# Performance work log

Hardware: AMD Instinct MI355X
Metric: run time of the kernel (lower is better)

Reference implementation:

```python
import jax, jax.numpy as jnp
from jax import lax
import numpy as np

# dims: T turns per dialogue, B dialogues, H = inpt_size (utter hidden), UE user embed,
# PE position embed, S = conv feature size, DEG avg in-degree
T, B, H, UE, PE, DEG = 30, 512, 256, 10, 16, 8
S = H + UE + PE          # 282, GRUCell(size, size)
OUT = 256                # context_hidden_size (output_size of linear2)
N = B * T                # merged graph nodes
E = N * DEG              # merged graph edges
LN_EPS = 1e-5


def _gru_cell(x, h, wih, whh, bih, bhh):
    # torch nn.GRUCell gate order: r, z, n
    gx = x @ wih.T + bih
    gh = h @ whh.T + bhh
    xr, xz, xn = jnp.split(gx, 3, axis=-1)
    hr, hz, hn = jnp.split(gh, 3, axis=-1)
    r = jax.nn.sigmoid(xr + hr)
    z = jax.nn.sigmoid(xz + hz)
    n = jnp.tanh(xn + r * hn)
    return (1.0 - z) * n + z * h


def _run_gru(xs, wih, whh, bih, bhh, reverse):
    # xs: [T, B, Din]; torch nn.GRU with zero initial hidden
    h0 = jnp.zeros((xs.shape[1], whh.shape[1]), xs.dtype)
    def step(h, x):
        hn = _gru_cell(x, h, wih, whh, bih, bhh)
        return hn, hn
    hT, ys = lax.scan(step, h0, xs, reverse=reverse)
    return ys, hT


def _forward(utter_hidden, ub, edge_weight,
             wih_f, whh_f, bih_f, bhh_f, wih_b, whh_b, bih_b, bhh_b,
             lin1_w, lin1_b, posemb,
             c1_wih, c1_whh, c1_bih, c1_bhh,
             c2_wih, c2_whh, c2_bih, c2_bhh,
             g1_w, g1_b, g2_w, g2_b, g3_w, g3_b,
             ln_g, ln_b, lin2_w, lin2_b, edge_index):
    # --- bidirectional GRU over turns + linear1 (GatedGCNContext.rnn) ---
    inp = jnp.concatenate([utter_hidden, ub], axis=-1)        # [T, B, H+UE]
    ys_f, h_f = _run_gru(inp, wih_f, whh_f, bih_f, bhh_f, False)
    ys_b, h_b = _run_gru(inp, wih_b, whh_b, bih_b, bhh_b, True)
    rnn_x = jnp.tanh(jnp.concatenate([ys_f, ys_b], -1) @ lin1_w.T + lin1_b)  # [T,B,H]
    # --- merged graph node features (PyG batching is batch-major) ---
    x0 = rnn_x.transpose(1, 0, 2).reshape(N, H)               # node b*T+t
    pos = posemb[jnp.tile(jnp.arange(T), B)]                  # [N, PE]
    ub_flat = ub.reshape(-1, UE)                              # faithful to original (turn-major)
    cell1 = (c1_wih, c1_whh, c1_bih, c1_bhh)
    cell2 = (c2_wih, c2_whh, c2_bih, c2_bhh)
    src, dst = edge_index[0], edge_index[1]

    def conv(xin, gw, gb):
        # message: edge_weight * GRUCell1(x_j, x_i); aggregate: scatter-add; update: Linear(GRUCell2(aggr, x))
        m = edge_weight[:, None] * _gru_cell(xin[src], xin[dst], *cell1)   # [E, S]
        aggr = jax.ops.segment_sum(m, dst, num_segments=N)                 # [N, S]
        return _gru_cell(aggr, xin, *cell2) @ gw.T + gb                    # [N, H]

    x1 = jnp.tanh(conv(jnp.concatenate([x0, pos, ub_flat], 1), g1_w, g1_b))
    x2 = jnp.tanh(conv(jnp.concatenate([x1, pos, ub_flat], 1), g2_w, g2_b))
    x3 = jnp.tanh(conv(jnp.concatenate([x2, pos, ub_flat], 1), g3_w, g3_b))
    xs = jnp.tanh(x1 + x2 + x3)
    mu = xs.mean(-1, keepdims=True)
    var = ((xs - mu) ** 2).mean(-1, keepdims=True)
    xs = ln_g * (xs - mu) / jnp.sqrt(var + LN_EPS) + ln_b     # LayerNorm (dropout = eval identity)
    gx = xs.reshape(B, T, H).transpose(1, 0, 2)               # chunk+stack+permute -> [T, B, H]
    out = jnp.tanh(jnp.concatenate([rnn_x, gx], -1) @ lin2_w.T + lin2_b)   # [T, B, OUT]
    return out


def setup_inputs() -> dict:
    key = jax.random.key(0)
    ks = iter(jax.random.split(key, 40))
    def p(shape):
        return jax.random.normal(next(ks), shape, dtype=jnp.float32) * 0.05
    # block-diagonal batched graph: per dialogue b, each node t receives DEG random in-edges
    rng = np.random.default_rng(0)
    off = (np.arange(B) * T)[:, None, None]
    src = rng.integers(0, T, size=(B, T, DEG)) + off
    dst = np.broadcast_to(np.arange(T)[None, :, None], (B, T, DEG)) + off
    edge_index = jnp.asarray(np.stack([src.ravel(), dst.ravel()]), dtype=jnp.int32)
    return {
        "utter_hidden": jax.random.normal(next(ks), (T, B, H), jnp.float32),
        "ub": jax.random.normal(next(ks), (T, B, UE), jnp.float32),
        "edge_weight": jax.random.uniform(next(ks), (E,), jnp.float32),
        "wih_f": p((3 * H, H + UE)), "whh_f": p((3 * H, H)), "bih_f": jnp.zeros((3 * H,)), "bhh_f": jnp.zeros((3 * H,)),
        "wih_b": p((3 * H, H + UE)), "whh_b": p((3 * H, H)), "bih_b": jnp.zeros((3 * H,)), "bhh_b": jnp.zeros((3 * H,)),
        "lin1_w": p((H, 2 * H)), "lin1_b": jnp.zeros((H,)),
        "posemb": p((100, PE)),
        "c1_wih": p((3 * S, S)), "c1_whh": p((3 * S, S)), "c1_bih": jnp.zeros((3 * S,)), "c1_bhh": jnp.zeros((3 * S,)),
        "c2_wih": p((3 * S, S)), "c2_whh": p((3 * S, S)), "c2_bih": jnp.zeros((3 * S,)), "c2_bhh": jnp.zeros((3 * S,)),
        "g1_w": p((H, S)), "g1_b": jnp.zeros((H,)),
        "g2_w": p((H, S)), "g2_b": jnp.zeros((H,)),
        "g3_w": p((H, S)), "g3_b": jnp.zeros((H,)),
        "ln_g": jnp.ones((H,)), "ln_b": jnp.zeros((H,)),
        "lin2_w": p((OUT, 2 * H)), "lin2_b": jnp.zeros((OUT,)),
        "edge_index": edge_index,
    }


def reference(utter_hidden, ub, edge_weight,
              wih_f, whh_f, bih_f, bhh_f, wih_b, whh_b, bih_b, bhh_b,
              lin1_w, lin1_b, posemb,
              c1_wih, c1_whh, c1_bih, c1_bhh,
              c2_wih, c2_whh, c2_bih, c2_bhh,
              g1_w, g1_b, g2_w, g2_b, g3_w, g3_b,
              ln_g, ln_b, lin2_w, lin2_b, edge_index):
    return _forward(utter_hidden, ub, edge_weight,
                    wih_f, whh_f, bih_f, bhh_f, wih_b, whh_b, bih_b, bhh_b,
                    lin1_w, lin1_b, posemb,
                    c1_wih, c1_whh, c1_bih, c1_bhh,
                    c2_wih, c2_whh, c2_bih, c2_bhh,
                    g1_w, g1_b, g2_w, g2_b, g3_w, g3_b,
                    ln_g, ln_b, lin2_w, lin2_b, edge_index)
```

## Files before the change

kernel.cpp:

```cpp
#include <hip/hip_runtime.h>
#include <math.h>

#define T_DIM 30
#define B_DIM 512
#define S_DIM 282
#define NB (T_DIM*B_DIM)
#define E_DIM (NB*8)
#define G3 846
#define GST 2538
#define KXP 288

typedef __attribute__((ext_vector_type(8))) short bf16x8;
typedef __attribute__((ext_vector_type(4))) float f32x4;

__device__ __forceinline__ float sigm(float x){ return 1.f/(1.f+expf(-x)); }

__device__ __forceinline__ ushort f2b(float f){
  union { float f; unsigned u; } v; v.f = f;
  unsigned r = v.u + 0x7fffu + ((v.u >> 16) & 1u);
  return (ushort)(r >> 16);
}
__device__ __forceinline__ float b2f(ushort b){
  union { unsigned u; float f; } v; v.u = ((unsigned)b) << 16; return v.f;
}
__device__ __forceinline__ void f2b2(float v, ushort& hi, ushort& lo){
  hi = f2b(v);
  lo = f2b(v - b2f(hi));
}

#define GLDS16(g, l) __builtin_amdgcn_global_load_lds( \
    (const __attribute__((address_space(1))) void*)(g), \
    (__attribute__((address_space(3))) void*)(l), 16, 0, 0)

__global__ __launch_bounds__(256, 2) void mfma_gemm3(
    const ushort* __restrict__ A, const ushort* __restrict__ W,
    const float* __restrict__ bias, float* __restrict__ C,
    int Nreal, int Kp, int ldc, int act, ushort* __restrict__ xout)
{
  __shared__ char smem[65536];

  int gx = gridDim.x;
  int h = blockIdx.y*gx + blockIdx.x;
  int nwg = gx*gridDim.y;
  int bx, by;
  if ((nwg & 7) == 0) {
    int q = nwg >> 3;
    int lwg = (h & 7)*q + (h >> 3);
    by = lwg / gx; bx = lwg - by*gx;
  } else { by = blockIdx.y; bx = blockIdx.x; }

  int tid  = threadIdx.x;
  int w    = tid >> 6;
  int lane = tid & 63;
  int lr = lane & 15;
  int lk = lane >> 4;
  int row0 = by*128;
  int col0 = bx*128;
  size_t astr = 2*(size_t)Kp;
  int NK = Kp >> 5;

  auto stage = [&](int buf, int kt){
    int kk = kt*32;
    char* Ab = smem + buf*32768;
    char* Wb = Ab + 16384;
    #pragma unroll
    for (int i = 0; i < 4; ++i) {
      int sb = w*256 + i*64;
      int s  = sb + lane;
      int r  = s >> 3;
      int rl = (s & 7) ^ (r & 7);
      int p  = rl >> 2, ks = rl & 3;
      const ushort* ga = A + (size_t)(row0 + r)*astr + (size_t)p*Kp + kk + ks*8;
      GLDS16(ga, Ab + sb*16);
      const ushort* gw = W + (size_t)(col0 + r)*astr + (size_t)p*Kp + kk + ks*8;
      GLDS16(gw, Wb + sb*16);
    }
  };
  auto rdfrag = [&](char* base, int r, int p)->bf16x8{
    int byte = r*128 + (((p*64) + lk*16) ^ ((r & 7) << 4));
    return *reinterpret_cast<const bf16x8*>(base + byte);
  };

  f32x4 acc[2][8] = {};
  stage(0, 0);
  __syncthreads();

  for (int kt = 0; kt < NK; ++kt) {
    int cur = kt & 1;
    if (kt + 1 < NK) stage(cur ^ 1, kt + 1);
    char* Ab = smem + cur*32768;
    char* Wb = Ab + 16384;

    bf16x8 a[2][2], b[8][2];
    #pragma unroll
    for (int i = 0; i < 2; ++i)
      #pragma unroll
      for (int p = 0; p < 2; ++p)
        a[i][p] = rdfrag(Ab, w*32 + i*16 + lr, p);
    #pragma unroll
    for (int j = 0; j < 8; ++j)
      #pragma unroll
      for (int p = 0; p < 2; ++p)
        b[j][p] = rdfrag(Wb, j*16 + lr, p);

    #pragma unroll
    for (int j = 0; j < 8; ++j) {
      acc[0][j] = __builtin_amdgcn_mfma_f32_16x16x32_bf16(a[0][0], b[j][0], acc[0][j], 0,0,0);
      acc[0][j] = __builtin_amdgcn_mfma_f32_16x16x32_bf16(a[0][1], b[j][0], acc[0][j], 0,0,0);
      acc[0][j] = __builtin_amdgcn_mfma_f32_16x16x32_bf16(a[0][0], b[j][1], acc[0][j], 0,0,0);
      acc[1][j] = __builtin_amdgcn_mfma_f32_16x16x32_bf16(a[1][0], b[j][0], acc[1][j], 0,0,0);
      acc[1][j] = __builtin_amdgcn_mfma_f32_16x16x32_bf16(a[1][1], b[j][0], acc[1][j], 0,0,0);
      acc[1][j] = __builtin_amdgcn_mfma_f32_16x16x32_bf16(a[1][0], b[j][1], acc[1][j], 0,0,0);
    }
    __syncthreads();
  }

  #pragma unroll
  for (int i = 0; i < 2; ++i) {
    #pragma unroll
    for (int j = 0; j < 8; ++j) {
      int cc = col0 + j*16 + lr;
      if (cc >= Nreal) continue;
      float bv = bias[cc];
      #pragma unroll
      for (int r = 0; r < 4; ++r) {
        int rr = row0 + w*32 + i*16 + lk*4 + r;
        float v = acc[i][j][r] + bv;
        if (act) v = tanhf(v);
        C[(size_t)rr*ldc + cc] = v;
        if (xout && cc < 256) {
          ushort hi, lo; f2b2(v, hi, lo);
          xout[(size_t)rr*2*KXP + cc]       = hi;
          xout[(size_t)rr*2*KXP + KXP + cc] = lo;
        }
      }
    }
  }
}

static inline void mgemm3(const ushort* A, const ushort* W, const float* bias,
                          float* C, int Nreal, int Npad, int Kp, int ldc,
                          int act, ushort* xout, hipStream_t s)
{
  dim3 grid((Npad + 127)/128, NB/128);
  mfma_gemm3<<<grid, 256, 0, s>>>(A, W, bias, C, Nreal, Kp, ldc, act, xout);
}

__global__ void cast_w(const float* __restrict__ w, ushort* __restrict__ wb,
                       int Nreal, int K, int Kp, int Npad)
{
  int idx = blockIdx.x*256 + threadIdx.x;
  if (idx >= Npad*Kp) return;
  int n = idx / Kp, k = idx - n*Kp;
  float v = (n < Nreal && k < K) ? w[(size_t)n*K + k] : 0.f;
  ushort hi, lo; f2b2(v, hi, lo);
  wb[(size_t)n*2*Kp + k]      = hi;
  wb[(size_t)n*2*Kp + Kp + k] = lo;
}
static inline void castw(const float* w, ushort* wb, int Nreal, int K, int Kp,
                         int Npad, hipStream_t s)
{
  int tot = Npad*Kp;
  cast_w<<<(tot+255)/256, 256, 0, s>>>(w, wb, Nreal, K, Kp, Npad);
}

__global__ void copy_f(const float* __restrict__ s, float* __restrict__ d, int n)
{
  int i = blockIdx.x*256 + threadIdx.x;
  if (i < n) d[i] = s[i];
}

__global__ void transpose_whh(const float* __restrict__ w, float* __restrict__ wt)
{
  int idx = blockIdx.x*256 + threadIdx.x;
  if (idx < 768*256) { int r = idx >> 8, c = idx & 255; wt[c*768 + r] = w[idx]; }
}

__global__ void build_inp(const float* __restrict__ utter, const float* __restrict__ ub,
                          ushort* __restrict__ inp)
{
  int r = blockIdx.x;
  for (int c = threadIdx.x; c < KXP; c += 128){
    float v = 0.f;
    if (c < 256)      v = utter[(size_t)r*256 + c];
    else if (c < 266) v = ub[(size_t)r*10 + (c-256)];
    ushort hi, lo; f2b2(v, hi, lo);
    inp[(size_t)r*2*KXP + c]       = hi;
    inp[(size_t)r*2*KXP + KXP + c] = lo;
  }
}

__global__ __launch_bounds__(256) void gru_step(
    const float* __restrict__ gx,
    const float* __restrict__ wtf, const float* __restrict__ bhh_f,
    const float* __restrict__ wtb, const float* __restrict__ bhh_b,
    float* __restrict__ ys_f, float* __restrict__ ys_b, int t)
{
  int dir = blockIdx.z;
  const float* wt  = dir ? wtb  : wtf;
  const float* bhh = dir ? bhh_b : bhh_f;
  float* ys = dir ? ys_b : ys_f;
  int tt = dir ? (T_DIM-1 - t) : t;
  const float* hprev = nullptr;
  if (t > 0) hprev = ys + (size_t)(dir ? tt+1 : tt-1) * B_DIM * 256;

  int tx = threadIdx.x & 63;
  int ty = threadIdx.x >> 6;
  int j = blockIdx.x * 64 + tx;
  int b = blockIdx.y * 4 + ty;

  __shared__ float sh[4][256];
  for (int i = threadIdx.x; i < 4*256; i += 256) {
    int bb = i >> 8, kk = i & 255;
    int gb = blockIdx.y*4 + bb;
    sh[bb][kk] = hprev ? hprev[(size_t)gb*256 + kk] : 0.f;
  }
  __syncthreads();

  float ar = bhh[j], az = bhh[256+j], an = bhh[512+j];
  for (int k = 0; k < 256; ++k) {
    float h = sh[ty][k];
    const float* wk = wt + (size_t)k*768;
    ar += h * wk[j];
    az += h * wk[256+j];
    an += h * wk[512+j];
  }
  size_t base = ((size_t)tt*B_DIM + b)*1536 + (size_t)dir*768;
  float r = sigm(gx[base + j]       + ar);
  float z = sigm(gx[base + 256 + j] + az);
  float n = tanhf(gx[base + 512 + j] + r*an);
  float h = sh[ty][j];
  ys[((size_t)tt*B_DIM + b)*256 + j] = (1.f - z)*n + z*h;
}

__global__ void build_cat(const float* __restrict__ a, const float* __restrict__ b2,
                          ushort* __restrict__ c, int mapmode)
{
  int r = blockIdx.x;
  int r2 = r;
  if (mapmode){ int t = r >> 9, bb = r & 511; r2 = bb*T_DIM + t; }
  for (int cix = threadIdx.x; cix < 512; cix += 128){
    float v = (cix < 256) ? a[(size_t)r*256 + cix] : b2[(size_t)r2*256 + (cix-256)];
    ushort hi, lo; f2b2(v, hi, lo);
    c[(size_t)r*1024 + cix]       = hi;
    c[(size_t)r*1024 + 512 + cix] = lo;
  }
}

__global__ void build_xin(const float* __restrict__ xsrc, int reorder,
                          const float* __restrict__ posemb, const float* __restrict__ ub,
                          ushort* __restrict__ xin)
{
  int n = blockIdx.x;
  int b = n / T_DIM, t = n % T_DIM;
  int srow = reorder ? (t*B_DIM + b) : n;
  for (int s = threadIdx.x; s < KXP; s += 128){
    float v = 0.f;
    if (s < 256)      v = xsrc[(size_t)srow*256 + s];
    else if (s < 272) v = posemb[t*16 + (s-256)];
    else if (s < 282) v = ub[(size_t)n*10 + (s-272)];
    ushort hi, lo; f2b2(v, hi, lo);
    xin[(size_t)n*2*KXP + s]       = hi;
    xin[(size_t)n*2*KXP + KXP + s] = lo;
  }
}

__global__ __launch_bounds__(128) void edge_aggr(
    const float* __restrict__ gate, const ushort* __restrict__ xin,
    const int* __restrict__ esrc, const int* __restrict__ edst,
    const float* __restrict__ ew, ushort* __restrict__ aggr)
{
  int e0 = blockIdx.x * 8;
  __shared__ int ssrc[8]; __shared__ float sw[8]; __shared__ int sdst;
  if (threadIdx.x < 8) { ssrc[threadIdx.x] = esrc[e0+threadIdx.x]; sw[threadIdx.x] = ew[e0+threadIdx.x]; }
  if (threadIdx.x == 0) sdst = edst[e0];
  __syncthreads();
  int i = sdst;
  for (int s = threadIdx.x; s < KXP; s += 128) {
    if (s >= S_DIM) {
      aggr[(size_t)i*2*KXP + s] = 0; aggr[(size_t)i*2*KXP + KXP + s] = 0; continue;
    }
    size_t gi = (size_t)i*GST;
    float hr = gate[gi + 846 + s];
    float hz = gate[gi + 1128 + s];
    float hn = gate[gi + 1410 + s];
    float hv = b2f(xin[(size_t)i*2*KXP + s]) + b2f(xin[(size_t)i*2*KXP + KXP + s]);
    float acc = 0.f;
    #pragma unroll
    for (int d = 0; d < 8; ++d) {
      size_t gj = (size_t)ssrc[d]*GST; float w = sw[d];
      float xr = gate[gj + s];
      float xz = gate[gj + 282 + s];
      float xn = gate[gj + 564 + s];
      float r = sigm(xr + hr);
      float z = sigm(xz + hz);
      float n = tanhf(xn + r*hn);
      acc += w * ((1.f - z)*n + z*hv);
    }
    ushort hi, lo; f2b2(acc, hi, lo);
    aggr[(size_t)i*2*KXP + s]       = hi;
    aggr[(size_t)i*2*KXP + KXP + s] = lo;
  }
}

__global__ __launch_bounds__(128) void gru2_combine(
    const float* __restrict__ gate, const ushort* __restrict__ xin,
    ushort* __restrict__ upd)
{
  int n = blockIdx.x;
  for (int s = threadIdx.x; s < KXP; s += 128) {
    if (s >= S_DIM) {
      upd[(size_t)n*2*KXP + s] = 0; upd[(size_t)n*2*KXP + KXP + s] = 0; continue;
    }
    size_t g = (size_t)n*GST;
    float xr = gate[g + 846 + s];
    float xz = gate[g + 1128 + s];
    float xn = gate[g + 1410 + s];
    float hr = gate[g + 1692 + s];
    float hz = gate[g + 1974 + s];
    float hn = gate[g + 2256 + s];
    float h  = b2f(xin[(size_t)n*2*KXP + s]) + b2f(xin[(size_t)n*2*KXP + KXP + s]);
    float r = sigm(xr + hr);
    float z = sigm(xz + hz);
    float nn = tanhf(xn + r*hn);
    ushort hi, lo; f2b2((1.f - z)*nn + z*h, hi, lo);
    upd[(size_t)n*2*KXP + s]       = hi;
    upd[(size_t)n*2*KXP + KXP + s] = lo;
  }
}

__global__ __launch_bounds__(256) void sum_ln(
    const float* __restrict__ x1, const float* __restrict__ x2, const float* __restrict__ x3,
    const float* __restrict__ g, const float* __restrict__ bta, float* __restrict__ out)
{
  int n = blockIdx.x; int j = threadIdx.x;
  size_t idx = (size_t)n*256 + j;
  float v = tanhf(x1[idx] + x2[idx] + x3[idx]);
  float s = v, sq = v*v;
  #pragma unroll
  for (int o = 32; o; o >>= 1) { s += __shfl_down(s, o, 64); sq += __shfl_down(sq, o, 64); }
  __shared__ float wsm[4], ws2[4];
  int lane = j & 63, w = j >> 6;
  if (lane == 0){ wsm[w] = s; ws2[w] = sq; }
  __syncthreads();
  float mean = (wsm[0]+wsm[1]+wsm[2]+wsm[3]) * (1.f/256.f);
  float m2   = (ws2[0]+ws2[1]+ws2[2]+ws2[3]) * (1.f/256.f);
  float var = m2 - mean*mean;
  float inv = rsqrtf(var + 1e-5f);
  out[idx] = g[j]*(v-mean)*inv + bta[j];
}

extern "C" void kernel_launch(void* const* d_in, const int* in_sizes, int n_in,
                              void* d_out, int out_size, void* d_ws, size_t ws_size,
                              hipStream_t stream)
{
  const float* utter = (const float*)d_in[0];
  const float* ub    = (const float*)d_in[1];
  const float* ew    = (const float*)d_in[2];
  const float* wih_f = (const float*)d_in[3];
  const float* whh_f = (const float*)d_in[4];
  const float* bih_f = (const float*)d_in[5];
  const float* bhh_f = (const float*)d_in[6];
  const float* wih_b = (const float*)d_in[7];
  const float* whh_b = (const float*)d_in[8];
  const float* bih_b = (const float*)d_in[9];
  const float* bhh_b = (const float*)d_in[10];
  const float* lin1_w= (const float*)d_in[11];
  const float* lin1_b= (const float*)d_in[12];
  const float* posemb= (const float*)d_in[13];
  const float* c1_wih= (const float*)d_in[14];
  const float* c1_whh= (const float*)d_in[15];
  const float* c1_bih= (const float*)d_in[16];
  const float* c1_bhh= (const float*)d_in[17];
  const float* c2_wih= (const float*)d_in[18];
  const float* c2_whh= (const float*)d_in[19];
  const float* c2_bih= (const float*)d_in[20];
  const float* c2_bhh= (const float*)d_in[21];
  const float* gw[3] = {(const float*)d_in[22], (const float*)d_in[24], (const float*)d_in[26]};
  const float* gb[3] = {(const float*)d_in[23], (const float*)d_in[25], (const float*)d_in[27]};
  const float* ln_g  = (const float*)d_in[28];
  const float* ln_b  = (const float*)d_in[29];
  const float* lin2_w= (const float*)d_in[30];
  const float* lin2_b= (const float*)d_in[31];
  const int*   eidx  = (const int*)d_in[32];
  const int* esrc = eidx;
  const int* edst = eidx + E_DIM;
  (void)ws_size; (void)n_in; (void)in_sizes; (void)out_size;

  float* ws = (float*)d_ws;
  size_t o = 0;
  auto A  = [&](size_t n){ size_t r = o; o += (n+3)&~(size_t)3; return r; };
  auto AU = [&](size_t n){ return A((n+1)/2); };

  size_t bGATE = A((size_t)NB*GST);
  size_t bYF   = A((size_t)NB*256);
  size_t bYB   = A((size_t)NB*256);
  size_t bRNN  = A((size_t)NB*256);
  size_t bBT   = A(2560);
  size_t bBX   = A(1536);
  size_t bB2   = A(896);
  size_t uXIN = AU((size_t)NB*2*KXP);
  size_t uAGG = AU((size_t)NB*2*KXP);
  size_t uWC1 = AU((size_t)2560*2*KXP);
  size_t uWXP = AU((size_t)1536*2*KXP);
  size_t uW2X = AU((size_t)896*2*KXP);
  size_t uG0  = AU((size_t)256*2*KXP);
  size_t uG1  = AU((size_t)256*2*KXP);
  size_t uG2  = AU((size_t)256*2*KXP);
  size_t uL1  = AU((size_t)256*2*512);
  size_t uL2  = AU((size_t)256*2*512);

  ushort* us = (ushort*)d_ws;
  auto U = [&](size_t fo){ return us + fo*2; };
  float* gate = ws + bGATE;
  float* wtf = gate + 23592960;
  float* wtb = wtf + 196608;
  ushort* uINP  = (ushort*)(ws + bYF);
  ushort* uCAT  = (ushort*)gate;
  float*  x3    = gate;

  castw(wih_f,  U(uWXP),                       768, 266,  KXP, 768, stream);
  castw(wih_b,  U(uWXP) + (size_t)768*2*KXP,   768, 266,  KXP, 768, stream);
  castw(c1_wih, U(uWC1),                       846, S_DIM, KXP, 846, stream);
  castw(c1_whh, U(uWC1) + (size_t)846*2*KXP,   846, S_DIM, KXP, 846, stream);
  castw(c2_whh, U(uWC1) + (size_t)1692*2*KXP,  846, S_DIM, KXP, 868, stream);
  castw(c2_wih, U(uW2X),                       846, S_DIM, KXP, 896, stream);
  castw(gw[0],  U(uG0), 256, S_DIM, KXP, 256, stream);
  castw(gw[1],  U(uG1), 256, S_DIM, KXP, 256, stream);
  castw(gw[2],  U(uG2), 256, S_DIM, KXP, 256, stream);
  castw(lin1_w, U(uL1), 256, 512, 512, 256, stream);
  castw(lin2_w, U(uL2), 256, 512, 512, 256, stream);
  const ushort* uGW[3] = {U(uG0), U(uG1), U(uG2)};
  copy_f<<<(846+255)/256,256,0,stream>>>(c1_bih, ws+bBT,        846);
  copy_f<<<(846+255)/256,256,0,stream>>>(c1_bhh, ws+bBT+846,    846);
  copy_f<<<(846+255)/256,256,0,stream>>>(c2_bhh, ws+bBT+1692,   846);
  copy_f<<<(768+255)/256,256,0,stream>>>(bih_f,  ws+bBX,        768);
  copy_f<<<(768+255)/256,256,0,stream>>>(bih_b,  ws+bBX+768,    768);
  copy_f<<<(846+255)/256,256,0,stream>>>(c2_bih, ws+bB2,        846);

  transpose_whh<<<(768*256+255)/256, 256, 0, stream>>>(whh_f, wtf);
  transpose_whh<<<(768*256+255)/256, 256, 0, stream>>>(whh_b, wtb);
  build_inp<<<NB, 128, 0, stream>>>(utter, ub, uINP);
  mgemm3(uINP, U(uWXP), ws+bBX, gate, 1536, 1536, KXP, 1536, 0, nullptr, stream);
  for (int t = 0; t < T_DIM; ++t)
    gru_step<<<dim3(4,128,2), 256, 0, stream>>>(gate, wtf, bhh_f, wtb, bhh_b,
                                                ws+bYF, ws+bYB, t);
  build_cat<<<NB, 128, 0, stream>>>(ws+bYF, ws+bYB, uCAT, 0);
  mgemm3(uCAT, U(uL1), lin1_b, ws+bRNN, 256, 256, 512, 256, 1, nullptr, stream);

  build_xin<<<NB, 128, 0, stream>>>(ws+bRNN, 1, posemb, ub, U(uXIN));
  float* XL[3] = {ws+bYF, ws+bYB, x3};
  for (int l = 0; l < 3; ++l) {
    mgemm3(U(uXIN), U(uWC1), ws+bBT, gate, 2538, 2560, KXP, GST, 0, nullptr, stream);
    edge_aggr<<<NB, 128, 0, stream>>>(gate, U(uXIN), esrc, edst, ew, U(uAGG));
    mgemm3(U(uAGG), U(uW2X), ws+bB2, gate + 846, 846, 896, KXP, GST, 0, nullptr, stream);
    gru2_combine<<<NB, 128, 0, stream>>>(gate, U(uXIN), U(uAGG));
    mgemm3(U(uAGG), uGW[l], gb[l], XL[l], 256, 256, KXP, 256, 1,
           (l < 2) ? U(uXIN) : nullptr, stream);
  }

  sum_ln<<<NB, 256, 0, stream>>>(XL[0], XL[1], XL[2], ln_g, ln_b, ws+bYF);
  build_cat<<<NB, 128, 0, stream>>>(ws+bRNN, ws+bYF, uCAT, 1);
  mgemm3(uCAT, U(uL2), lin2_b, (float*)d_out, 256, 256, 512, 256, 1, nullptr, stream);
}
```

Measured before the change: 1.923 ms.

## Stream GEMM weights from global, restructure GRU step, merge bias copies, swizzle edge order

The MFMA GEMM now stages only the A tile in LDS, halving shared memory so more blocks fit per CU, and loads W fragments straight from global/L2 inside the k-loop. The recurrent GRU step reads whh in its original row-major layout with float4 dot products, and each block now covers 32 batch rows and 8 gate columns. That removes the transpose kernels. The six bias copy launches become one kernel, and edge_aggr remaps node order across blocks to spread memory access. Direct global W loads in the GEMM inner loop risk latency stalls that LDS staging used to hide.

```diff
diff --git a/kernel.cpp b/kernel.cpp
--- a/kernel.cpp
+++ b/kernel.cpp
@@ -32,12 +32,12 @@
     (const __attribute__((address_space(1))) void*)(g), \
     (__attribute__((address_space(3))) void*)(l), 16, 0, 0)
 
-__global__ __launch_bounds__(256, 2) void mfma_gemm3(
+__global__ __launch_bounds__(256, 4) void mfma_gemm4(
     const ushort* __restrict__ A, const ushort* __restrict__ W,
     const float* __restrict__ bias, float* __restrict__ C,
     int Nreal, int Kp, int ldc, int act, ushort* __restrict__ xout)
 {
-  __shared__ char smem[65536];
+  __shared__ char smem[32768];
 
   int gx = gridDim.x;
   int h = blockIdx.y*gx + blockIdx.x;
@@ -59,10 +59,9 @@
   size_t astr = 2*(size_t)Kp;
   int NK = Kp >> 5;
 
-  auto stage = [&](int buf, int kt){
+  auto stageA = [&](int buf, int kt){
     int kk = kt*32;
-    char* Ab = smem + buf*32768;
-    char* Wb = Ab + 16384;
+    char* Ab = smem + buf*16384;
     #pragma unroll
     for (int i = 0; i < 4; ++i) {
       int sb = w*256 + i*64;
@@ -72,8 +71,6 @@
       int p  = rl >> 2, ks = rl & 3;
       const ushort* ga = A + (size_t)(row0 + r)*astr + (size_t)p*Kp + kk + ks*8;
       GLDS16(ga, Ab + sb*16);
-      const ushort* gw = W + (size_t)(col0 + r)*astr + (size_t)p*Kp + kk + ks*8;
-      GLDS16(gw, Wb + sb*16);
     }
   };
   auto rdfrag = [&](char* base, int r, int p)->bf16x8{
@@ -82,35 +79,33 @@
   };
 
   f32x4 acc[2][8] = {};
-  stage(0, 0);
+  stageA(0, 0);
   __syncthreads();
 
   for (int kt = 0; kt < NK; ++kt) {
     int cur = kt & 1;
-    if (kt + 1 < NK) stage(cur ^ 1, kt + 1);
-    char* Ab = smem + cur*32768;
-    char* Wb = Ab + 16384;
-
-    bf16x8 a[2][2], b[8][2];
+    if (kt + 1 < NK) stageA(cur ^ 1, kt + 1);
+    char* Ab = smem + cur*16384;
+    int kk = kt*32;
+
+    bf16x8 a[2][2];
     #pragma unroll
     for (int i = 0; i < 2; ++i)
       #pragma unroll
       for (int p = 0; p < 2; ++p)
         a[i][p] = rdfrag(Ab, w*32 + i*16 + lr, p);
-    #pragma unroll
-    for (int j = 0; j < 8; ++j)
-      #pragma unroll
-      for (int p = 0; p < 2; ++p)
-        b[j][p] = rdfrag(Wb, j*16 + lr, p);
 
     #pragma unroll
     for (int j = 0; j < 8; ++j) {
-      acc[0][j] = __builtin_amdgcn_mfma_f32_16x16x32_bf16(a[0][0], b[j][0], acc[0][j], 0,0,0);
-      acc[0][j] = __builtin_amdgcn_mfma_f32_16x16x32_bf16(a[0][1], b[j][0], acc[0][j], 0,0,0);
-      acc[0][j] = __builtin_amdgcn_mfma_f32_16x16x32_bf16(a[0][0], b[j][1], acc[0][j], 0,0,0);
-      acc[1][j] = __builtin_amdgcn_mfma_f32_16x16x32_bf16(a[1][0], b[j][0], acc[1][j], 0,0,0);
-      acc[1][j] = __builtin_amdgcn_mfma_f32_16x16x32_bf16(a[1][1], b[j][0], acc[1][j], 0,0,0);
-      acc[1][j] = __builtin_amdgcn_mfma_f32_16x16x32_bf16(a[1][0], b[j][1], acc[1][j], 0,0,0);
+      const ushort* wp = W + (size_t)(col0 + j*16 + lr)*astr + kk + lk*8;
+      bf16x8 bh = *reinterpret_cast<const bf16x8*>(wp);
+      bf16x8 bl = *reinterpret_cast<const bf16x8*>(wp + Kp);
+      acc[0][j] = __builtin_amdgcn_mfma_f32_16x16x32_bf16(a[0][0], bh, acc[0][j], 0,0,0);
+      acc[0][j] = __builtin_amdgcn_mfma_f32_16x16x32_bf16(a[0][1], bh, acc[0][j], 0,0,0);
+      acc[0][j] = __builtin_amdgcn_mfma_f32_16x16x32_bf16(a[0][0], bl, acc[0][j], 0,0,0);
+      acc[1][j] = __builtin_amdgcn_mfma_f32_16x16x32_bf16(a[1][0], bh, acc[1][j], 0,0,0);
+      acc[1][j] = __builtin_amdgcn_mfma_f32_16x16x32_bf16(a[1][1], bh, acc[1][j], 0,0,0);
+      acc[1][j] = __builtin_amdgcn_mfma_f32_16x16x32_bf16(a[1][0], bl, acc[1][j], 0,0,0);
     }
     __syncthreads();
   }
@@ -138,12 +133,12 @@
   }
 }
 
-static inline void mgemm3(const ushort* A, const ushort* W, const float* bias,
+static inline void mgemm4(const ushort* A, const ushort* W, const float* bias,
                           float* C, int Nreal, int Npad, int Kp, int ldc,
                           int act, ushort* xout, hipStream_t s)
 {
   dim3 grid((Npad + 127)/128, NB/128);
-  mfma_gemm3<<<grid, 256, 0, s>>>(A, W, bias, C, Nreal, Kp, ldc, act, xout);
+  mfma_gemm4<<<grid, 256, 0, s>>>(A, W, bias, C, Nreal, Kp, ldc, act, xout);
 }
 
 __global__ void cast_w(const float* __restrict__ w, ushort* __restrict__ wb,
@@ -164,16 +159,17 @@
   cast_w<<<(tot+255)/256, 256, 0, s>>>(w, wb, Nreal, K, Kp, Npad);
 }
 
-__global__ void copy_f(const float* __restrict__ s, float* __restrict__ d, int n)
+__global__ void copy_bias(const float* __restrict__ c1_bih, const float* __restrict__ c1_bhh,
+                          const float* __restrict__ c2_bhh, const float* __restrict__ bih_f,
+                          const float* __restrict__ bih_b, const float* __restrict__ c2_bih,
+                          float* __restrict__ bt, float* __restrict__ bx, float* __restrict__ b2)
 {
   int i = blockIdx.x*256 + threadIdx.x;
-  if (i < n) d[i] = s[i];
-}
-
-__global__ void transpose_whh(const float* __restrict__ w, float* __restrict__ wt)
-{
-  int idx = blockIdx.x*256 + threadIdx.x;
-  if (idx < 768*256) { int r = idx >> 8, c = idx & 255; wt[c*768 + r] = w[idx]; }
+  if (i < 846) {
+    bt[i] = c1_bih[i]; bt[846+i] = c1_bhh[i]; bt[1692+i] = c2_bhh[i];
+    b2[i] = c2_bih[i];
+  }
+  if (i < 768) { bx[i] = bih_f[i]; bx[768+i] = bih_b[i]; }
 }
 
 __global__ void build_inp(const float* __restrict__ utter, const float* __restrict__ ub,
@@ -190,46 +186,51 @@
   }
 }
 
-__global__ __launch_bounds__(256) void gru_step(
+__global__ __launch_bounds__(256) void gru_step2(
     const float* __restrict__ gx,
-    const float* __restrict__ wtf, const float* __restrict__ bhh_f,
-    const float* __restrict__ wtb, const float* __restrict__ bhh_b,
+    const float* __restrict__ whh_f, const float* __restrict__ bhh_f,
+    const float* __restrict__ whh_b, const float* __restrict__ bhh_b,
     float* __restrict__ ys_f, float* __restrict__ ys_b, int t)
 {
   int dir = blockIdx.z;
-  const float* wt  = dir ? wtb  : wtf;
+  const float* wh  = dir ? whh_b : whh_f;
   const float* bhh = dir ? bhh_b : bhh_f;
   float* ys = dir ? ys_b : ys_f;
   int tt = dir ? (T_DIM-1 - t) : t;
-  const float* hprev = nullptr;
-  if (t > 0) hprev = ys + (size_t)(dir ? tt+1 : tt-1) * B_DIM * 256;
-
-  int tx = threadIdx.x & 63;
-  int ty = threadIdx.x >> 6;
-  int j = blockIdx.x * 64 + tx;
-  int b = blockIdx.y * 4 + ty;
-
-  __shared__ float sh[4][256];
-  for (int i = threadIdx.x; i < 4*256; i += 256) {
-    int bb = i >> 8, kk = i & 255;
-    int gb = blockIdx.y*4 + bb;
-    sh[bb][kk] = hprev ? hprev[(size_t)gb*256 + kk] : 0.f;
+  const float* hprev = (t > 0) ? ys + (size_t)(dir ? tt+1 : tt-1)*B_DIM*256 : nullptr;
+
+  int jg = threadIdx.x & 7;
+  int bb = threadIdx.x >> 3;
+  int j  = blockIdx.x*8 + jg;
+  int b  = blockIdx.y*32 + bb;
+
+  __shared__ float sh[32][260];
+  for (int i = threadIdx.x; i < 32*256; i += 256) {
+    int ib = i >> 8, kk = i & 255;
+    int gb = blockIdx.y*32 + ib;
+    sh[ib][kk] = hprev ? hprev[(size_t)gb*256 + kk] : 0.f;
   }
   __syncthreads();
 
+  const float* wr = wh + (size_t)j*256;
+  const float* wz = wh + (size_t)(256+j)*256;
+  const float* wn = wh + (size_t)(512+j)*256;
   float ar = bhh[j], az = bhh[256+j], an = bhh[512+j];
-  for (int k = 0; k < 256; ++k) {
-    float h = sh[ty][k];
-    const float* wk = wt + (size_t)k*768;
-    ar += h * wk[j];
-    az += h * wk[256+j];
-    an += h * wk[512+j];
+  #pragma unroll 4
+  for (int k = 0; k < 256; k += 4) {
+    float4 h4 = *reinterpret_cast<const float4*>(&sh[bb][k]);
+    float4 r4 = *reinterpret_cast<const float4*>(wr + k);
+    float4 z4 = *reinterpret_cast<const float4*>(wz + k);
+    float4 n4 = *reinterpret_cast<const float4*>(wn + k);
+    ar += h4.x*r4.x + h4.y*r4.y + h4.z*r4.z + h4.w*r4.w;
+    az += h4.x*z4.x + h4.y*z4.y + h4.z*z4.z + h4.w*z4.w;
+    an += h4.x*n4.x + h4.y*n4.y + h4.z*n4.z + h4.w*n4.w;
   }
   size_t base = ((size_t)tt*B_DIM + b)*1536 + (size_t)dir*768;
   float r = sigm(gx[base + j]       + ar);
   float z = sigm(gx[base + 256 + j] + az);
   float n = tanhf(gx[base + 512 + j] + r*an);
-  float h = sh[ty][j];
+  float h = sh[bb][j];
   ys[((size_t)tt*B_DIM + b)*256 + j] = (1.f - z)*n + z*h;
 }
 
@@ -270,7 +271,9 @@
     const int* __restrict__ esrc, const int* __restrict__ edst,
     const float* __restrict__ ew, ushort* __restrict__ aggr)
 {
-  int e0 = blockIdx.x * 8;
+  int bid = blockIdx.x;
+  int node = (bid & 7)*(NB/8) + (bid >> 3);
+  int e0 = node * 8;
   __shared__ int ssrc[8]; __shared__ float sw[8]; __shared__ int sdst;
   if (threadIdx.x < 8) { ssrc[threadIdx.x] = esrc[e0+threadIdx.x]; sw[threadIdx.x] = ew[e0+threadIdx.x]; }
   if (threadIdx.x == 0) sdst = edst[e0];
@@ -413,8 +416,6 @@
   ushort* us = (ushort*)d_ws;
   auto U = [&](size_t fo){ return us + fo*2; };
   float* gate = ws + bGATE;
-  float* wtf = gate + 23592960;
-  float* wtb = wtf + 196608;
   ushort* uINP  = (ushort*)(ws + bYF);
   ushort* uCAT  = (ushort*)gate;
   float*  x3    = gate;
@@ -431,35 +432,29 @@
   castw(lin1_w, U(uL1), 256, 512, 512, 256, stream);
   castw(lin2_w, U(uL2), 256, 512, 512, 256, stream);
   const ushort* uGW[3] = {U(uG0), U(uG1), U(uG2)};
-  copy_f<<<(846+255)/256,256,0,stream>>>(c1_bih, ws+bBT,        846);
-  copy_f<<<(846+255)/256,256,0,stream>>>(c1_bhh, ws+bBT+846,    846);
-  copy_f<<<(846+255)/256,256,0,stream>>>(c2_bhh, ws+bBT+1692,   846);
-  copy_f<<<(768+255)/256,256,0,stream>>>(bih_f,  ws+bBX,        768);
-  copy_f<<<(768+255)/256,256,0,stream>>>(bih_b,  ws+bBX+768,    768);
-  copy_f<<<(846+255)/256,256,0,stream>>>(c2_bih, ws+bB2,        846);
-
-  transpose_whh<<<(768*256+255)/256, 256, 0, stream>>>(whh_f, wtf);
-  transpose_whh<<<(768*256+255)/256, 256, 0, stream>>>(whh_b, wtb);
+  copy_bias<<<4, 256, 0, stream>>>(c1_bih, c1_bhh, c2_bhh, bih_f, bih_b, c2_bih,
+                                   ws+bBT, ws+bBX, ws+bB2);
+
   build_inp<<<NB, 128, 0, stream>>>(utter, ub, uINP);
-  mgemm3(uINP, U(uWXP), ws+bBX, gate, 1536, 1536, KXP, 1536, 0, nullptr, stream);
+  mgemm4(uINP, U(uWXP), ws+bBX, gate, 1536, 1536, KXP, 1536, 0, nullptr, stream);
   for (int t = 0; t < T_DIM; ++t)
-    gru_step<<<dim3(4,128,2), 256, 0, stream>>>(gate, wtf, bhh_f, wtb, bhh_b,
-                                                ws+bYF, ws+bYB, t);
+    gru_step2<<<dim3(32,16,2), 256, 0, stream>>>(gate, whh_f, bhh_f, whh_b, bhh_b,
+                                                 ws+bYF, ws+bYB, t);
   build_cat<<<NB, 128, 0, stream>>>(ws+bYF, ws+bYB, uCAT, 0);
-  mgemm3(uCAT, U(uL1), lin1_b, ws+bRNN, 256, 256, 512, 256, 1, nullptr, stream);
+  mgemm4(uCAT, U(uL1), lin1_b, ws+bRNN, 256, 256, 512, 256, 1, nullptr, stream);
 
   build_xin<<<NB, 128, 0, stream>>>(ws+bRNN, 1, posemb, ub, U(uXIN));
   float* XL[3] = {ws+bYF, ws+bYB, x3};
   for (int l = 0; l < 3; ++l) {
-    mgemm3(U(uXIN), U(uWC1), ws+bBT, gate, 2538, 2560, KXP, GST, 0, nullptr, stream);
+    mgemm4(U(uXIN), U(uWC1), ws+bBT, gate, 2538, 2560, KXP, GST, 0, nullptr, stream);
     edge_aggr<<<NB, 128, 0, stream>>>(gate, U(uXIN), esrc, edst, ew, U(uAGG));
-    mgemm3(U(uAGG), U(uW2X), ws+bB2, gate + 846, 846, 896, KXP, GST, 0, nullptr, stream);
+    mgemm4(U(uAGG), U(uW2X), ws+bB2, gate + 846, 846, 896, KXP, GST, 0, nullptr, stream);
     gru2_combine<<<NB, 128, 0, stream>>>(gate, U(uXIN), U(uAGG));
-    mgemm3(U(uAGG), uGW[l], gb[l], XL[l], 256, 256, KXP, 256, 1,
+    mgemm4(U(uAGG), uGW[l], gb[l], XL[l], 256, 256, KXP, 256, 1,
            (l < 2) ? U(uXIN) : nullptr, stream);
   }
 
   sum_ln<<<NB, 256, 0, stream>>>(XL[0], XL[1], XL[2], ln_g, ln_b, ws+bYF);
   build_cat<<<NB, 128, 0, stream>>>(ws+bRNN, ws+bYF, uCAT, 1);
-  mgemm3(uCAT, U(uL2), lin2_b, (float*)d_out, 256, 256, 512, 256, 1, nullptr, stream);
-}
+  mgemm4(uCAT, U(uL2), lin2_b, (float*)d_out, 256, 256, 512, 256, 1, nullptr, stream);
+}
```

After: 4.816 ms. 150% more time.
